# Kernel tuning notes

Measured on AMD Instinct MI355X. Metric: run time of the kernel, lower is better.

Reference implementation:

```python
import jax, jax.numpy as jnp
import numpy as np

N_I = 500_000   # 'indivi' nodes (dst)
N_H = 200_000   # 'house' nodes
F_I = 32        # indivi feature dim
F_H = 16        # house feature dim
EF = 8          # edge_attr dim
E1 = 2_000_000  # house->indivi edges
E2 = 2_000_000  # indivi->indivi edges


def setup_inputs() -> dict:
    key = jax.random.key(0)
    ks = jax.random.split(key, 16)
    return {
        "x_indivi": jax.random.normal(ks[0], (N_I, F_I), jnp.float32),
        "x_house": jax.random.normal(ks[1], (N_H, F_H), jnp.float32),
        "edge_attr_h2i": jax.random.normal(ks[2], (E1, EF), jnp.float32),
        "edge_attr_i2i": jax.random.normal(ks[3], (E2, EF), jnp.float32),
        "W_edge_h2i": jax.random.normal(ks[4], (F_H, EF), jnp.float32) * 0.1,
        "b_edge_h2i": jax.random.normal(ks[5], (F_H,), jnp.float32) * 0.1,
        "W_edge_i2i": jax.random.normal(ks[6], (F_I, EF), jnp.float32) * 0.1,
        "b_edge_i2i": jax.random.normal(ks[7], (F_I,), jnp.float32) * 0.1,
        "W_root_h2i": jax.random.normal(ks[8], (1, F_I), jnp.float32) * 0.1,
        "bias_h2i": jax.random.normal(ks[9], (1,), jnp.float32) * 0.1,
        "W_root_i2i": jax.random.normal(ks[10], (1, F_I), jnp.float32) * 0.1,
        "bias_i2i": jax.random.normal(ks[11], (1,), jnp.float32) * 0.1,
        "src_h2i": jax.random.randint(ks[12], (E1,), 0, N_H, jnp.int32),
        "dst_h2i": jax.random.randint(ks[13], (E1,), 0, N_I, jnp.int32),
        "src_i2i": jax.random.randint(ks[14], (E2,), 0, N_I, jnp.int32),
        "dst_i2i": jax.random.randint(ks[15], (E2,), 0, N_I, jnp.int32),
    }


def _nnconv(x_src, x_dst, edge_attr, src, dst, W_edge, b_edge, W_root, bias, num_dst):
    # Edge MLP -> per-edge weight matrix of shape [F_src, out=1], flattened to [E, F_src]
    w = edge_attr @ W_edge.T + b_edge                     # [E, F_src]
    # message_e = x_src[src_e] @ w_e  (out_channels = 1)
    msg = jnp.sum(x_src[src] * w, axis=-1, keepdims=True)  # [E, 1]
    agg = jax.ops.segment_sum(msg, dst, num_segments=num_dst)  # [N_dst, 1]
    # root transform on destination features + bias
    return agg + x_dst @ W_root.T + bias                  # [N_dst, 1]


def reference(x_indivi, x_house, edge_attr_h2i, edge_attr_i2i,
              W_edge_h2i, b_edge_h2i, W_edge_i2i, b_edge_i2i,
              W_root_h2i, bias_h2i, W_root_i2i, bias_i2i,
              src_h2i, dst_h2i, src_i2i, dst_i2i):
    out_h = _nnconv(x_house, x_indivi, edge_attr_h2i, src_h2i, dst_h2i,
                    W_edge_h2i, b_edge_h2i, W_root_h2i, bias_h2i, N_I)
    out_i = _nnconv(x_indivi, x_indivi, edge_attr_i2i, src_i2i, dst_i2i,
                    W_edge_i2i, b_edge_i2i, W_root_i2i, bias_i2i, N_I)
    # HeteroConv(aggr='sum') over the two relations targeting 'indivi'
    return out_h + out_i
```

## Files before the change

### kernel.cpp

```cpp
#include <hip/hip_runtime.h>

#define N_I 500000
#define N_H 200000
#define E1  2000000
#define E2  2000000
#define TOTAL_E (E1 + E2)

#define NB 512
#define CHUNK 8192
#define NWG ((TOTAL_E + CHUNK - 1) / CHUNK)
#define NB_RED ((N_I + 1023) / 1024)

static_assert(NWG <= 512, "scan assumes <=512 workgroups");

template<int F, bool ROOT>
__global__ __launch_bounds__(256) void precompute_g(
    const float* __restrict__ x, const float* __restrict__ W, const float* __restrict__ b,
    float* __restrict__ g, int n,
    const float* __restrict__ rW1, const float* __restrict__ rW2,
    const float* __restrict__ rb1, const float* __restrict__ rb2,
    float* __restrict__ out)
{
    __shared__ float Wf[F * 8];
    __shared__ float bv[F];
    __shared__ float wr[F];

    for (int i = threadIdx.x; i < F * 8; i += 256) Wf[i] = W[i];
    if (threadIdx.x < F) {
        bv[threadIdx.x] = b[threadIdx.x];
        if (ROOT) wr[threadIdx.x] = rW1[threadIdx.x] + rW2[threadIdx.x];
    }
    __syncthreads();

    int nid = blockIdx.x * 256 + threadIdx.x;
    if (nid >= n) return;

    float xv[F];
    const float4* xp = (const float4*)(x + (size_t)nid * F);
    #pragma unroll
    for (int q = 0; q < F / 4; q++) {
        float4 v = xp[q];
        xv[q*4+0] = v.x; xv[q*4+1] = v.y; xv[q*4+2] = v.z; xv[q*4+3] = v.w;
    }

    float acc[9];
    #pragma unroll
    for (int k = 0; k < 9; k++) acc[k] = 0.f;

    #pragma unroll
    for (int j = 0; j < F; j++) {
        float4 w0 = *(const float4*)(Wf + j * 8);
        float4 w1 = *(const float4*)(Wf + j * 8 + 4);
        float xj = xv[j];
        acc[0] = fmaf(xj, w0.x, acc[0]);
        acc[1] = fmaf(xj, w0.y, acc[1]);
        acc[2] = fmaf(xj, w0.z, acc[2]);
        acc[3] = fmaf(xj, w0.w, acc[3]);
        acc[4] = fmaf(xj, w1.x, acc[4]);
        acc[5] = fmaf(xj, w1.y, acc[5]);
        acc[6] = fmaf(xj, w1.z, acc[6]);
        acc[7] = fmaf(xj, w1.w, acc[7]);
        acc[8] = fmaf(xj, bv[j], acc[8]);
    }

    float4* gp = (float4*)(g + (size_t)nid * 12);
    gp[0] = make_float4(acc[0], acc[1], acc[2], acc[3]);
    gp[1] = make_float4(acc[4], acc[5], acc[6], acc[7]);
    gp[2] = make_float4(acc[8], 0.f, 0.f, 0.f);

    if (ROOT) {
        float r = rb1[0] + rb2[0];
        #pragma unroll
        for (int j = 0; j < F; j++) r = fmaf(xv[j], wr[j], r);
        out[nid] = r;
    }
}

__device__ __forceinline__ void edge_msg(
    int t,
    const int* __restrict__ src1, const int* __restrict__ dst1,
    const float* __restrict__ ea1, const float* __restrict__ g1,
    const int* __restrict__ src2, const int* __restrict__ dst2,
    const float* __restrict__ ea2, const float* __restrict__ g2,
    int& d_out, float& m_out)
{
    const int* srcp; const int* dstp; const float* eap; const float* gp;
    int e;
    if (t < E1) { e = t;      srcp = src1; dstp = dst1; eap = ea1; gp = g1; }
    else        { e = t - E1; srcp = src2; dstp = dst2; eap = ea2; gp = g2; }

    int s = srcp[e];
    d_out = dstp[e];
    const float4* ap = (const float4*)(eap + (size_t)e * 8);
    float4 a0 = ap[0];
    float4 a1 = ap[1];
    const float4* gr = (const float4*)(gp + (size_t)s * 12);
    float4 ga = gr[0];
    float4 gb = gr[1];
    float4 gc = gr[2];

    float msg = gc.x;
    msg = fmaf(a0.x, ga.x, msg);
    msg = fmaf(a0.y, ga.y, msg);
    msg = fmaf(a0.z, ga.z, msg);
    msg = fmaf(a0.w, ga.w, msg);
    msg = fmaf(a1.x, gb.x, msg);
    msg = fmaf(a1.y, gb.y, msg);
    msg = fmaf(a1.z, gb.z, msg);
    msg = fmaf(a1.w, gb.w, msg);
    m_out = msg;
}

__global__ __launch_bounds__(256) void msg_hist_kernel(
    const int* __restrict__ src1, const int* __restrict__ dst1,
    const float* __restrict__ ea1, const float* __restrict__ g1,
    const int* __restrict__ src2, const int* __restrict__ dst2,
    const float* __restrict__ ea2, const float* __restrict__ g2,
    float* __restrict__ msg_out, int* __restrict__ H)
{
    __shared__ int hist[NB];
    for (int i = threadIdx.x; i < NB; i += 256) hist[i] = 0;
    __syncthreads();

    int base = blockIdx.x * CHUNK;
    #pragma unroll 2
    for (int it = 0; it < CHUNK / 256; ++it) {
        int t = base + it * 256 + threadIdx.x;
        if (t < TOTAL_E) {
            int d; float m;
            edge_msg(t, src1, dst1, ea1, g1, src2, dst2, ea2, g2, d, m);
            msg_out[t] = m;
            atomicAdd(&hist[d >> 10], 1);
        }
    }
    __syncthreads();
    for (int i = threadIdx.x; i < NB; i += 256) H[blockIdx.x * NB + i] = hist[i];
}

__global__ __launch_bounds__(512) void scan_cols_kernel(int* __restrict__ H,
                                                        int* __restrict__ total)
{
    __shared__ int v[512];
    int b = blockIdx.x;
    int tid = threadIdx.x;
    int orig = (tid < NWG) ? H[tid * NB + b] : 0;
    v[tid] = orig;
    __syncthreads();
    for (int off = 1; off < 512; off <<= 1) {
        int t = (tid >= off) ? v[tid - off] : 0;
        __syncthreads();
        v[tid] += t;
        __syncthreads();
    }
    if (tid < NWG) H[tid * NB + b] = v[tid] - orig;
    if (tid == 511) total[b] = v[511];
}

__global__ __launch_bounds__(512) void scan_base_kernel(const int* __restrict__ total,
                                                        int* __restrict__ base)
{
    __shared__ int v[512];
    int tid = threadIdx.x;
    int orig = total[tid];
    v[tid] = orig;
    __syncthreads();
    for (int off = 1; off < 512; off <<= 1) {
        int t = (tid >= off) ? v[tid - off] : 0;
        __syncthreads();
        v[tid] += t;
        __syncthreads();
    }
    base[tid] = v[tid] - orig;
}

__global__ __launch_bounds__(256) void scatter_kernel(
    const int* __restrict__ dst1, const int* __restrict__ dst2,
    const float* __restrict__ msg, const int* __restrict__ H,
    const int* __restrict__ base, uint2* __restrict__ pairs)
{
    __shared__ int cur[NB];
    for (int i = threadIdx.x; i < NB; i += 256)
        cur[i] = H[blockIdx.x * NB + i] + base[i];
    __syncthreads();

    int cbase = blockIdx.x * CHUNK;
    #pragma unroll 2
    for (int it = 0; it < CHUNK / 256; ++it) {
        int t = cbase + it * 256 + threadIdx.x;
        if (t < TOTAL_E) {
            int d = (t < E1) ? dst1[t] : dst2[t - E1];
            float m = msg[t];
            int pos = atomicAdd(&cur[d >> 10], 1);
            pairs[pos] = make_uint2((unsigned)d, __float_as_uint(m));
        }
    }
}

__global__ __launch_bounds__(256) void reduce_kernel(
    const uint2* __restrict__ pairs, const int* __restrict__ base,
    const int* __restrict__ total, float* __restrict__ out)
{
    __shared__ float acc[1024];
    for (int i = threadIdx.x; i < 1024; i += 256) acc[i] = 0.f;
    __syncthreads();

    int b = blockIdx.x;
    int start = base[b];
    int cnt = total[b];
    for (int i = threadIdx.x; i < cnt; i += 256) {
        uint2 p = pairs[start + i];
        atomicAdd(&acc[p.x & 1023], __uint_as_float(p.y));
    }
    __syncthreads();

    int nb = b << 10;
    for (int i = threadIdx.x; i < 1024; i += 256) {
        int n = nb + i;
        if (n < N_I) out[n] += acc[i];
    }
}

__global__ __launch_bounds__(256) void edge_kernel_atomic(
    const int* __restrict__ src1, const int* __restrict__ dst1,
    const float* __restrict__ ea1, const float* __restrict__ g1,
    const int* __restrict__ src2, const int* __restrict__ dst2,
    const float* __restrict__ ea2, const float* __restrict__ g2,
    float* __restrict__ out)
{
    int t = blockIdx.x * 256 + threadIdx.x;
    if (t >= TOTAL_E) return;
    int d; float m;
    edge_msg(t, src1, dst1, ea1, g1, src2, dst2, ea2, g2, d, m);
    atomicAdd(out + d, m);
}

extern "C" void kernel_launch(void* const* d_in, const int* in_sizes, int n_in,
                              void* d_out, int out_size, void* d_ws, size_t ws_size,
                              hipStream_t stream) {
    const float* x_i  = (const float*)d_in[0];
    const float* x_h  = (const float*)d_in[1];
    const float* ea_h = (const float*)d_in[2];
    const float* ea_i = (const float*)d_in[3];
    const float* We_h = (const float*)d_in[4];
    const float* be_h = (const float*)d_in[5];
    const float* We_i = (const float*)d_in[6];
    const float* be_i = (const float*)d_in[7];
    const float* Wr_h = (const float*)d_in[8];
    const float* br_h = (const float*)d_in[9];
    const float* Wr_i = (const float*)d_in[10];
    const float* br_i = (const float*)d_in[11];
    const int* src_h = (const int*)d_in[12];
    const int* dst_h = (const int*)d_in[13];
    const int* src_i = (const int*)d_in[14];
    const int* dst_i = (const int*)d_in[15];

    float* out = (float*)d_out;

    char* ws = (char*)d_ws;
    float* g_i = (float*)ws;
    float* g_h = (float*)(ws + 24000000);
    float* msg = (float*)(ws + 33600000);
    int*   H   = (int*)  (ws + 49600000);
    int*   tot = (int*)  (ws + 50603008);
    int*   bas = (int*)  (ws + 50605056);
    uint2* pairs = (uint2*)ws;
    const size_t WS_NEEDED = 50607104;

    precompute_g<16, false><<<(N_H + 255) / 256, 256, 0, stream>>>(
        x_h, We_h, be_h, g_h, N_H, nullptr, nullptr, nullptr, nullptr, nullptr);
    precompute_g<32, true><<<(N_I + 255) / 256, 256, 0, stream>>>(
        x_i, We_i, be_i, g_i, N_I, Wr_h, Wr_i, br_h, br_i, out);

    if (ws_size >= WS_NEEDED) {
        msg_hist_kernel<<<NWG, 256, 0, stream>>>(
            src_h, dst_h, ea_h, g_h, src_i, dst_i, ea_i, g_i, msg, H);
        scan_cols_kernel<<<NB, 512, 0, stream>>>(H, tot);
        scan_base_kernel<<<1, 512, 0, stream>>>(tot, bas);
        scatter_kernel<<<NWG, 256, 0, stream>>>(
            dst_h, dst_i, msg, H, bas, pairs);
        reduce_kernel<<<NB_RED, 256, 0, stream>>>(pairs, bas, tot, out);
    } else {
        edge_kernel_atomic<<<(TOTAL_E + 255) / 256, 256, 0, stream>>>(
            src_h, dst_h, ea_h, g_h, src_i, dst_i, ea_i, g_i, out);
    }
}
```

Measured before the change: 384.9 us.

## Move message computation into scatter pass; histogram only dst indices

The histogram pass now reads only destination indices. Message computation moves into the scatter kernel, which writes (dst, msg) pairs directly. This drops the intermediate msg array's write and re-read, and pairs get their own workspace region. The chunk size shrinks to 2048, giving more workgroups, so the column scan now handles up to 2048 entries per thread block with 8 values per thread. The reduce kernel uses 1024 threads per block. The workspace requirement grows, which risks falling back to the atomic path if the harness provides less.

Result: slower. 443.3 us (+15.2%).

```diff
diff --git a/kernel.cpp b/kernel.cpp
--- a/kernel.cpp
+++ b/kernel.cpp
@@ -7,11 +7,10 @@
 #define TOTAL_E (E1 + E2)
 
 #define NB 512
-#define CHUNK 8192
+#define CHUNK 2048
 #define NWG ((TOTAL_E + CHUNK - 1) / CHUNK)
 #define NB_RED ((N_I + 1023) / 1024)
-
-static_assert(NWG <= 512, "scan assumes <=512 workgroups");
+#define WPT 8
 
 template<int F, bool ROOT>
 __global__ __launch_bounds__(256) void precompute_g(
@@ -111,113 +110,122 @@
     m_out = msg;
 }
 
-__global__ __launch_bounds__(256) void msg_hist_kernel(
+__global__ __launch_bounds__(256) void hist_kernel(
+    const int* __restrict__ dst1, const int* __restrict__ dst2,
+    int* __restrict__ H)
+{
+    __shared__ int hist[NB];
+    for (int i = threadIdx.x; i < NB; i += 256) hist[i] = 0;
+    __syncthreads();
+
+    int base = blockIdx.x * CHUNK;
+    #pragma unroll
+    for (int it = 0; it < CHUNK / 256; ++it) {
+        int t = base + it * 256 + threadIdx.x;
+        if (t < TOTAL_E) {
+            int d = (t < E1) ? dst1[t] : dst2[t - E1];
+            atomicAdd(&hist[d >> 10], 1);
+        }
+    }
+    __syncthreads();
+    for (int i = threadIdx.x; i < NB; i += 256) H[blockIdx.x * NB + i] = hist[i];
+}
+
+__global__ __launch_bounds__(256) void scan_cols_kernel(int* __restrict__ H,
+                                                        int* __restrict__ total)
+{
+    __shared__ int sums[256];
+    int b = blockIdx.x;
+    int tid = threadIdx.x;
+
+    int vals[WPT];
+    int s = 0;
+    #pragma unroll
+    for (int k = 0; k < WPT; k++) {
+        int w = tid * WPT + k;
+        vals[k] = (w < NWG) ? H[w * NB + b] : 0;
+        s += vals[k];
+    }
+    sums[tid] = s;
+    __syncthreads();
+    for (int off = 1; off < 256; off <<= 1) {
+        int t = (tid >= off) ? sums[tid - off] : 0;
+        __syncthreads();
+        sums[tid] += t;
+        __syncthreads();
+    }
+    int run = sums[tid] - s;
+    #pragma unroll
+    for (int k = 0; k < WPT; k++) {
+        int w = tid * WPT + k;
+        if (w < NWG) H[w * NB + b] = run;
+        run += vals[k];
+    }
+    if (tid == 255) total[b] = sums[255];
+}
+
+__global__ __launch_bounds__(512) void scan_base_kernel(const int* __restrict__ total,
+                                                        int* __restrict__ base)
+{
+    __shared__ int v[512];
+    int tid = threadIdx.x;
+    int orig = total[tid];
+    v[tid] = orig;
+    __syncthreads();
+    for (int off = 1; off < 512; off <<= 1) {
+        int t = (tid >= off) ? v[tid - off] : 0;
+        __syncthreads();
+        v[tid] += t;
+        __syncthreads();
+    }
+    base[tid] = v[tid] - orig;
+}
+
+__global__ __launch_bounds__(256) void scatter_msg_kernel(
     const int* __restrict__ src1, const int* __restrict__ dst1,
     const float* __restrict__ ea1, const float* __restrict__ g1,
     const int* __restrict__ src2, const int* __restrict__ dst2,
     const float* __restrict__ ea2, const float* __restrict__ g2,
-    float* __restrict__ msg_out, int* __restrict__ H)
-{
-    __shared__ int hist[NB];
-    for (int i = threadIdx.x; i < NB; i += 256) hist[i] = 0;
-    __syncthreads();
-
-    int base = blockIdx.x * CHUNK;
-    #pragma unroll 2
+    const int* __restrict__ H, const int* __restrict__ base,
+    uint2* __restrict__ pairs)
+{
+    __shared__ int cur[NB];
+    for (int i = threadIdx.x; i < NB; i += 256)
+        cur[i] = H[blockIdx.x * NB + i] + base[i];
+    __syncthreads();
+
+    int cbase = blockIdx.x * CHUNK;
+    #pragma unroll
     for (int it = 0; it < CHUNK / 256; ++it) {
-        int t = base + it * 256 + threadIdx.x;
+        int t = cbase + it * 256 + threadIdx.x;
         if (t < TOTAL_E) {
             int d; float m;
             edge_msg(t, src1, dst1, ea1, g1, src2, dst2, ea2, g2, d, m);
-            msg_out[t] = m;
-            atomicAdd(&hist[d >> 10], 1);
-        }
-    }
-    __syncthreads();
-    for (int i = threadIdx.x; i < NB; i += 256) H[blockIdx.x * NB + i] = hist[i];
-}
-
-__global__ __launch_bounds__(512) void scan_cols_kernel(int* __restrict__ H,
-                                                        int* __restrict__ total)
-{
-    __shared__ int v[512];
-    int b = blockIdx.x;
-    int tid = threadIdx.x;
-    int orig = (tid < NWG) ? H[tid * NB + b] : 0;
-    v[tid] = orig;
-    __syncthreads();
-    for (int off = 1; off < 512; off <<= 1) {
-        int t = (tid >= off) ? v[tid - off] : 0;
-        __syncthreads();
-        v[tid] += t;
-        __syncthreads();
-    }
-    if (tid < NWG) H[tid * NB + b] = v[tid] - orig;
-    if (tid == 511) total[b] = v[511];
-}
-
-__global__ __launch_bounds__(512) void scan_base_kernel(const int* __restrict__ total,
-                                                        int* __restrict__ base)
-{
-    __shared__ int v[512];
-    int tid = threadIdx.x;
-    int orig = total[tid];
-    v[tid] = orig;
-    __syncthreads();
-    for (int off = 1; off < 512; off <<= 1) {
-        int t = (tid >= off) ? v[tid - off] : 0;
-        __syncthreads();
-        v[tid] += t;
-        __syncthreads();
-    }
-    base[tid] = v[tid] - orig;
-}
-
-__global__ __launch_bounds__(256) void scatter_kernel(
-    const int* __restrict__ dst1, const int* __restrict__ dst2,
-    const float* __restrict__ msg, const int* __restrict__ H,
-    const int* __restrict__ base, uint2* __restrict__ pairs)
-{
-    __shared__ int cur[NB];
-    for (int i = threadIdx.x; i < NB; i += 256)
-        cur[i] = H[blockIdx.x * NB + i] + base[i];
-    __syncthreads();
-
-    int cbase = blockIdx.x * CHUNK;
-    #pragma unroll 2
-    for (int it = 0; it < CHUNK / 256; ++it) {
-        int t = cbase + it * 256 + threadIdx.x;
-        if (t < TOTAL_E) {
-            int d = (t < E1) ? dst1[t] : dst2[t - E1];
-            float m = msg[t];
             int pos = atomicAdd(&cur[d >> 10], 1);
             pairs[pos] = make_uint2((unsigned)d, __float_as_uint(m));
         }
     }
 }
 
-__global__ __launch_bounds__(256) void reduce_kernel(
+__global__ __launch_bounds__(1024) void reduce_kernel(
     const uint2* __restrict__ pairs, const int* __restrict__ base,
     const int* __restrict__ total, float* __restrict__ out)
 {
     __shared__ float acc[1024];
-    for (int i = threadIdx.x; i < 1024; i += 256) acc[i] = 0.f;
+    if (threadIdx.x < 1024) acc[threadIdx.x] = 0.f;
     __syncthreads();
 
     int b = blockIdx.x;
     int start = base[b];
     int cnt = total[b];
-    for (int i = threadIdx.x; i < cnt; i += 256) {
+    for (int i = threadIdx.x; i < cnt; i += 1024) {
         uint2 p = pairs[start + i];
         atomicAdd(&acc[p.x & 1023], __uint_as_float(p.y));
     }
     __syncthreads();
 
-    int nb = b << 10;
-    for (int i = threadIdx.x; i < 1024; i += 256) {
-        int n = nb + i;
-        if (n < N_I) out[n] += acc[i];
-    }
+    int n = (b << 10) + threadIdx.x;
+    if (n < N_I) out[n] += acc[threadIdx.x];
 }
 
 __global__ __launch_bounds__(256) void edge_kernel_atomic(
@@ -257,14 +265,13 @@
     float* out = (float*)d_out;
 
     char* ws = (char*)d_ws;
-    float* g_i = (float*)ws;
-    float* g_h = (float*)(ws + 24000000);
-    float* msg = (float*)(ws + 33600000);
-    int*   H   = (int*)  (ws + 49600000);
-    int*   tot = (int*)  (ws + 50603008);
-    int*   bas = (int*)  (ws + 50605056);
-    uint2* pairs = (uint2*)ws;
-    const size_t WS_NEEDED = 50607104;
+    float* g_i   = (float*)ws;
+    float* g_h   = (float*)(ws + 24000000);
+    uint2* pairs = (uint2*)(ws + 33600000);
+    int*   H     = (int*)  (ws + 65600000);
+    int*   tot   = (int*)  (ws + 69601792);
+    int*   bas   = (int*)  (ws + 69603840);
+    const size_t WS_NEEDED = 69605888;
 
     precompute_g<16, false><<<(N_H + 255) / 256, 256, 0, stream>>>(
         x_h, We_h, be_h, g_h, N_H, nullptr, nullptr, nullptr, nullptr, nullptr);
@@ -272,13 +279,12 @@
         x_i, We_i, be_i, g_i, N_I, Wr_h, Wr_i, br_h, br_i, out);
 
     if (ws_size >= WS_NEEDED) {
-        msg_hist_kernel<<<NWG, 256, 0, stream>>>(
-            src_h, dst_h, ea_h, g_h, src_i, dst_i, ea_i, g_i, msg, H);
-        scan_cols_kernel<<<NB, 512, 0, stream>>>(H, tot);
+        hist_kernel<<<NWG, 256, 0, stream>>>(dst_h, dst_i, H);
+        scan_cols_kernel<<<NB, 256, 0, stream>>>(H, tot);
         scan_base_kernel<<<1, 512, 0, stream>>>(tot, bas);
-        scatter_kernel<<<NWG, 256, 0, stream>>>(
-            dst_h, dst_i, msg, H, bas, pairs);
-        reduce_kernel<<<NB_RED, 256, 0, stream>>>(pairs, bas, tot, out);
+        scatter_msg_kernel<<<NWG, 256, 0, stream>>>(
+            src_h, dst_h, ea_h, g_h, src_i, dst_i, ea_i, g_i, H, bas, pairs);
+        reduce_kernel<<<NB_RED, 1024, 0, stream>>>(pairs, bas, tot, out);
     } else {
         edge_kernel_atomic<<<(TOTAL_E + 255) / 256, 256, 0, stream>>>(
             src_h, dst_h, ea_h, g_h, src_i, dst_i, ea_i, g_i, out);
```
